# Kernel tuning notes

Measured on AMD Instinct MI355X. Metric: run time of the kernel, lower is better.

## Reference

```python
import jax, jax.numpy as jnp
import numpy as np


def _trilinear_sample(src, flow):
    """Faithful port of VoxelMorph SpatialTransformer: identity grid + flow,
    trilinear grid_sample with align_corners=True and zero padding.
    Normalization to [-1,1] followed by grid_sample's un-normalization
    (align_corners=True) is the identity, so we sample directly at voxel
    coordinates grid + flow.  src: [B,C,D,H,W], flow: [B,3,D,H,W]."""
    B, C, D, H, W = src.shape
    gz, gy, gx = jnp.meshgrid(jnp.arange(D, dtype=src.dtype),
                              jnp.arange(H, dtype=src.dtype),
                              jnp.arange(W, dtype=src.dtype), indexing='ij')
    z = gz[None] + flow[:, 0]  # [B,D,H,W] sample coords along dim0
    y = gy[None] + flow[:, 1]
    x = gx[None] + flow[:, 2]

    z0 = jnp.floor(z); y0 = jnp.floor(y); x0 = jnp.floor(x)
    fz = z - z0; fy = y - y0; fx = x - x0
    z0i = z0.astype(jnp.int32); y0i = y0.astype(jnp.int32); x0i = x0.astype(jnp.int32)

    N = D * H * W
    src_flat = src.reshape(B, C, N)
    gather = jax.vmap(lambda sf, li: sf[:, li])  # per-batch gather over flat spatial

    out = jnp.zeros((B, C, N), dtype=src.dtype)
    for dz in (0, 1):
        wz = fz if dz else (1.0 - fz)
        zi = z0i + dz
        for dy in (0, 1):
            wy = fy if dy else (1.0 - fy)
            yi = y0i + dy
            for dx in (0, 1):
                wx = fx if dx else (1.0 - fx)
                xi = x0i + dx
                # zero padding: out-of-bounds corners contribute nothing
                valid = ((zi >= 0) & (zi < D) & (yi >= 0) & (yi < H) &
                         (xi >= 0) & (xi < W))
                zc = jnp.clip(zi, 0, D - 1)
                yc = jnp.clip(yi, 0, H - 1)
                xc = jnp.clip(xi, 0, W - 1)
                lin = ((zc * H + yc) * W + xc).reshape(B, N)
                w = (wz * wy * wx * valid.astype(src.dtype)).reshape(B, 1, N)
                out = out + w * gather(src_flat, lin)  # [B,C,N]
    return out.reshape(B, C, D, H, W)


def setup_inputs() -> dict:
    key = jax.random.key(0)
    k1, k2 = jax.random.split(key)
    src = jax.random.normal(k1, (2, 2, 160, 192, 160), dtype=jnp.float32)
    flow = jax.random.normal(k2, (2, 3, 160, 192, 160), dtype=jnp.float32)
    return {"src": src, "flow": flow}


def reference(src, flow):
    return _trilinear_sample(src, flow)
```

## Files before the change

kernel.cpp:

```cpp
#include <hip/hip_runtime.h>

#define BB 2
#define CC 2
#define DD 160
#define HH 192
#define WW 160
#define HW_ (HH * WW)
#define NN (DD * HW_)

#define TX 32
#define TY 8
#define CZ 20
#define HALO 4
#define SLOTS 10
#define ROWS (TY + 2 * HALO)
#define RSTR (TX + 2 * HALO)
#define PLANE_CH (RSTR * ROWS)
#define PLANE_LDS (PLANE_CH * CC)

typedef float f2u __attribute__((ext_vector_type(2), aligned(4)));

__global__ __launch_bounds__(256) void st_warp3d_tiled(
    const float* __restrict__ src,
    const float* __restrict__ flow,
    float* __restrict__ out)
{
    const int tid = threadIdx.x;
    const int tx = tid & (TX - 1);
    const int ty = tid >> 5;

    const int tile = blockIdx.x;
    const int Xo = (tile % 5) * TX;
    const int Yo = (tile / 5) * TY;
    const int Z0 = blockIdx.y * CZ;
    const int b  = blockIdx.z;

    const int x = Xo + tx;
    const int y = Yo + ty;

    const int sxlo = max(Xo - HALO, 0);
    const int sxhi = min(Xo + TX + HALO, WW);
    const int Ws   = sxhi - sxlo;
    const int sylo = max(Yo - HALO, 0);
    const int syhi = min(Yo + TY + HALO, HH);
    const int Rs   = syhi - sylo;

    __shared__ float lds[SLOTS * PLANE_LDS];

    const float* __restrict__ sbase = src + (size_t)b * CC * NN;

    int goffA = 0, loffA = 0; bool vA;
    {
        const int s  = tid;
        const int ch = (s >= 160) ? 1 : 0;
        const int r  = s - ch * 160;
        const int yy = r / 10;
        const int xs = r - yy * 10;
        vA    = (yy < Rs) && (xs * 4 < Ws);
        goffA = ch * NN + (sylo + yy) * WW + sxlo + xs * 4;
        loffA = ch * PLANE_CH + yy * RSTR + xs * 4;
    }
    int goffB = 0, loffB = 0; bool vB = false;
    if (tid < 64) {
        const int s  = tid + 256;
        const int r  = s - 160;
        const int yy = r / 10;
        const int xs = r - yy * 10;
        vB    = (yy < Rs) && (xs * 4 < Ws);
        goffB = NN + (sylo + yy) * WW + sxlo + xs * 4;
        loffB = PLANE_CH + yy * RSTR + xs * 4;
    }

    const int qlo  = max(Z0 - HALO, 0);
    const int qhi0 = min(Z0 + HALO, DD - 1);
    for (int qq = qlo; qq <= qhi0; ++qq) {
        const float* gp = sbase + (size_t)qq * HW_;
        float* lp = lds + (qq % SLOTS) * PLANE_LDS;
        if (vA) *(float4*)(lp + loffA) = *(const float4*)(gp + goffA);
        if (vB) *(float4*)(lp + loffB) = *(const float4*)(gp + goffB);
    }
    const int qmax = min(DD - 1, Z0 + CZ - 1 + HALO);

    const size_t fbase = (size_t)b * 3 * NN + (size_t)y * WW + x;
    const size_t obase = (size_t)b * CC * NN + (size_t)y * WW + x;

    for (int z = Z0; z < Z0 + CZ; ++z) {
        __syncthreads();

        const int qp = z + HALO + 1;
        const bool pre = (qp <= qmax);
        float4 pA, pB;
        if (pre) {
            const float* gp = sbase + (size_t)qp * HW_;
            if (vA) pA = *(const float4*)(gp + goffA);
            if (vB) pB = *(const float4*)(gp + goffB);
        }

        const float* fl = flow + fbase + (size_t)z * HW_;
        const float fzv = __builtin_nontemporal_load(fl);
        const float fyv = __builtin_nontemporal_load(fl + NN);
        const float fxv = __builtin_nontemporal_load(fl + 2 * (size_t)NN);
        const float zc = (float)z + fzv;
        const float yc = (float)y + fyv;
        const float xc = (float)x + fxv;

        const float z0f = floorf(zc), y0f = floorf(yc), x0f = floorf(xc);
        const float fz = zc - z0f, fy = yc - y0f, fx = xc - x0f;
        const int z0 = (int)z0f, y0 = (int)y0f, x0 = (int)x0f;
        const int z1 = z0 + 1, y1 = y0 + 1, x1 = x0 + 1;

        const float wz0 = (z0 >= 0 && z0 < DD) ? (1.0f - fz) : 0.0f;
        const float wz1 = (z1 >= 0 && z1 < DD) ? fz : 0.0f;
        const float wy0 = (y0 >= 0 && y0 < HH) ? (1.0f - fy) : 0.0f;
        const float wy1 = (y1 >= 0 && y1 < HH) ? fy : 0.0f;
        const float wx0 = (x0 >= 0 && x0 < WW) ? (1.0f - fx) : 0.0f;
        const float wx1 = (x1 >= 0 && x1 < WW) ? fx : 0.0f;

        const int z0c = min(max(z0, 0), DD - 1), z1c = min(max(z1, 0), DD - 1);
        const int y0c = min(max(y0, 0), HH - 1), y1c = min(max(y1, 0), HH - 1);
        const int x0c = min(max(x0, 0), WW - 1), x1c = min(max(x1, 0), WW - 1);
        const int xb  = min(max(x0, 0), WW - 2);

        const float q0 = (x0c == xb ? wx0 : 0.0f) + (x1c == xb ? wx1 : 0.0f);
        const float q1 = (wx0 + wx1) - q0;
        const float w00 = wz0 * wy0, w01 = wz0 * wy1, w10 = wz1 * wy0, w11 = wz1 * wy1;
        const float w00q0 = w00 * q0, w00q1 = w00 * q1;
        const float w01q0 = w01 * q0, w01q1 = w01 * q1;
        const float w10q0 = w10 * q0, w10q1 = w10 * q1;
        const float w11q0 = w11 * q0, w11q1 = w11 * q1;

        const int dzi = z0 - z, dyi = y0 - y, dxi = x0 - x;
        const bool inTile = ((unsigned)(dzi + HALO) <= 7u) &&
                            ((unsigned)(dyi + HALO) <= 7u) &&
                            ((unsigned)(dxi + HALO) <= 7u);

        float acc0, acc1;
        if (inTile) {
            const int slot0 = z0c % SLOTS;
            const int slot1 = z1c % SLOTS;
            const int yi0 = y0c - sylo, yi1 = y1c - sylo;
            const int xi  = xb - sxlo;
            const int i00 = slot0 * PLANE_LDS + yi0 * RSTR + xi;
            const int i01 = slot0 * PLANE_LDS + yi1 * RSTR + xi;
            const int i10 = slot1 * PLANE_LDS + yi0 * RSTR + xi;
            const int i11 = slot1 * PLANE_LDS + yi1 * RSTR + xi;

            const float a00x = lds[i00],            a00y = lds[i00 + 1];
            const float a01x = lds[i01],            a01y = lds[i01 + 1];
            const float a10x = lds[i10],            a10y = lds[i10 + 1];
            const float a11x = lds[i11],            a11y = lds[i11 + 1];
            const float b00x = lds[i00 + PLANE_CH], b00y = lds[i00 + PLANE_CH + 1];
            const float b01x = lds[i01 + PLANE_CH], b01y = lds[i01 + PLANE_CH + 1];
            const float b10x = lds[i10 + PLANE_CH], b10y = lds[i10 + PLANE_CH + 1];
            const float b11x = lds[i11 + PLANE_CH], b11y = lds[i11 + PLANE_CH + 1];

            acc0 = a00x * w00q0 + a00y * w00q1 + a01x * w01q0 + a01y * w01q1 +
                   a10x * w10q0 + a10y * w10q1 + a11x * w11q0 + a11y * w11q1;
            acc1 = b00x * w00q0 + b00y * w00q1 + b01x * w01q0 + b01y * w01q1 +
                   b10x * w10q0 + b10y * w10q1 + b11x * w11q0 + b11y * w11q1;
        } else {
            const int r00 = (z0c * HH + y0c) * WW + xb;
            const int r01 = (z0c * HH + y1c) * WW + xb;
            const int r10 = (z1c * HH + y0c) * WW + xb;
            const int r11 = (z1c * HH + y1c) * WW + xb;
            const float* s1p = sbase + NN;
            const f2u a00 = *(const f2u*)(sbase + r00);
            const f2u a01 = *(const f2u*)(sbase + r01);
            const f2u a10 = *(const f2u*)(sbase + r10);
            const f2u a11 = *(const f2u*)(sbase + r11);
            const f2u c00 = *(const f2u*)(s1p + r00);
            const f2u c01 = *(const f2u*)(s1p + r01);
            const f2u c10 = *(const f2u*)(s1p + r10);
            const f2u c11 = *(const f2u*)(s1p + r11);
            acc0 = a00.x * w00q0 + a00.y * w00q1 + a01.x * w01q0 + a01.y * w01q1 +
                   a10.x * w10q0 + a10.y * w10q1 + a11.x * w11q0 + a11.y * w11q1;
            acc1 = c00.x * w00q0 + c00.y * w00q1 + c01.x * w01q0 + c01.y * w01q1 +
                   c10.x * w10q0 + c10.y * w10q1 + c11.x * w11q0 + c11.y * w11q1;
        }

        float* o = out + obase + (size_t)z * HW_;
        __builtin_nontemporal_store(acc0, o);
        __builtin_nontemporal_store(acc1, o + NN);

        if (pre) {
            float* lp = lds + (qp % SLOTS) * PLANE_LDS;
            if (vA) *(float4*)(lp + loffA) = pA;
            if (vB) *(float4*)(lp + loffB) = pB;
        }
    }
}

extern "C" void kernel_launch(void* const* d_in, const int* in_sizes, int n_in,
                              void* d_out, int out_size, void* d_ws, size_t ws_size,
                              hipStream_t stream) {
    const float* src  = (const float*)d_in[0];
    const float* flow = (const float*)d_in[1];
    float* out = (float*)d_out;

    dim3 grid(5 * 24, DD / CZ, BB);
    dim3 block(256);
    st_warp3d_tiled<<<grid, block, 0, stream>>>(src, flow, out);
}
```

Measured before the change: 290.6 us.

## Enlarge tile to 32x16, use anisotropic halo, and deepen plane prefetch pipeline

Doubles the tile height to 16 rows with 512 threads, shrinks the Y halo to 3 while keeping X/Z halos at 4, and adds an extra LDS slot so the next source plane is written at the top of each iteration while the following plane is loaded into registers. The larger tile reduces halo overhead per output and the one-iteration-deeper prefetch hides global load latency across the barrier. The in-tile test is rewritten to compare against the actual loaded bounds, so samples with displacement beyond the smaller Y halo fall back to global gathers more often.

```diff
diff --git a/kernel.cpp b/kernel.cpp
--- a/kernel.cpp
+++ b/kernel.cpp
@@ -9,18 +9,20 @@
 #define NN (DD * HW_)
 
 #define TX 32
-#define TY 8
+#define TY 16
 #define CZ 20
-#define HALO 4
-#define SLOTS 10
-#define ROWS (TY + 2 * HALO)
-#define RSTR (TX + 2 * HALO)
+#define HX 4
+#define HY 3
+#define HZ 4
+#define SLOTS 11
+#define ROWS (TY + 2 * HY)
+#define RSTR (TX + 2 * HX)
 #define PLANE_CH (RSTR * ROWS)
 #define PLANE_LDS (PLANE_CH * CC)
 
 typedef float f2u __attribute__((ext_vector_type(2), aligned(4)));
 
-__global__ __launch_bounds__(256) void st_warp3d_tiled(
+__global__ __launch_bounds__(512, 4) void st_warp3d_tiled2(
     const float* __restrict__ src,
     const float* __restrict__ flow,
     float* __restrict__ out)
@@ -38,48 +40,38 @@
     const int x = Xo + tx;
     const int y = Yo + ty;
 
-    const int sxlo = max(Xo - HALO, 0);
-    const int sxhi = min(Xo + TX + HALO, WW);
+    const int sxlo = max(Xo - HX, 0);
+    const int sxhi = min(Xo + TX + HX, WW);
     const int Ws   = sxhi - sxlo;
-    const int sylo = max(Yo - HALO, 0);
-    const int syhi = min(Yo + TY + HALO, HH);
+    const int sylo = max(Yo - HY, 0);
+    const int syhi = min(Yo + TY + HY, HH);
     const int Rs   = syhi - sylo;
 
     __shared__ float lds[SLOTS * PLANE_LDS];
-
     const float* __restrict__ sbase = src + (size_t)b * CC * NN;
 
-    int goffA = 0, loffA = 0; bool vA;
+    int goff = 0, loff = 0; bool vA = false;
     {
-        const int s  = tid;
-        const int ch = (s >= 160) ? 1 : 0;
-        const int r  = s - ch * 160;
+        const int ch = tid >> 8;
+        const int r  = tid & 255;
         const int yy = r / 10;
         const int xs = r - yy * 10;
-        vA    = (yy < Rs) && (xs * 4 < Ws);
-        goffA = ch * NN + (sylo + yy) * WW + sxlo + xs * 4;
-        loffA = ch * PLANE_CH + yy * RSTR + xs * 4;
-    }
-    int goffB = 0, loffB = 0; bool vB = false;
-    if (tid < 64) {
-        const int s  = tid + 256;
-        const int r  = s - 160;
-        const int yy = r / 10;
-        const int xs = r - yy * 10;
-        vB    = (yy < Rs) && (xs * 4 < Ws);
-        goffB = NN + (sylo + yy) * WW + sxlo + xs * 4;
-        loffB = PLANE_CH + yy * RSTR + xs * 4;
+        vA   = (r < ROWS * 10) && (yy < Rs) && (xs * 4 < Ws);
+        goff = ch * NN + (sylo + yy) * WW + sxlo + xs * 4;
+        loff = ch * PLANE_CH + yy * RSTR + xs * 4;
     }
 
-    const int qlo  = max(Z0 - HALO, 0);
-    const int qhi0 = min(Z0 + HALO, DD - 1);
-    for (int qq = qlo; qq <= qhi0; ++qq) {
-        const float* gp = sbase + (size_t)qq * HW_;
-        float* lp = lds + (qq % SLOTS) * PLANE_LDS;
-        if (vA) *(float4*)(lp + loffA) = *(const float4*)(gp + goffA);
-        if (vB) *(float4*)(lp + loffB) = *(const float4*)(gp + goffB);
+    const int qmax = min(DD - 1, Z0 + CZ - 1 + HZ + 1);
+    for (int q = max(Z0 - HZ, 0); q <= min(Z0 + HZ + 1, DD - 1); ++q) {
+        if (vA) *(float4*)(lds + (q % SLOTS) * PLANE_LDS + loff) =
+                *(const float4*)(sbase + (size_t)q * HW_ + goff);
     }
-    const int qmax = min(DD - 1, Z0 + CZ - 1 + HALO);
+    float4 preg{};
+    {
+        const int p0 = Z0 + HZ + 2;
+        if (p0 <= qmax && vA)
+            preg = *(const float4*)(sbase + (size_t)p0 * HW_ + goff);
+    }
 
     const size_t fbase = (size_t)b * 3 * NN + (size_t)y * WW + x;
     const size_t obase = (size_t)b * CC * NN + (size_t)y * WW + x;
@@ -87,14 +79,13 @@
     for (int z = Z0; z < Z0 + CZ; ++z) {
         __syncthreads();
 
-        const int qp = z + HALO + 1;
-        const bool pre = (qp <= qmax);
-        float4 pA, pB;
-        if (pre) {
-            const float* gp = sbase + (size_t)qp * HW_;
-            if (vA) pA = *(const float4*)(gp + goffA);
-            if (vB) pB = *(const float4*)(gp + goffB);
-        }
+        const int wp = z + HZ + 2;
+        if (wp <= qmax && vA)
+            *(float4*)(lds + (wp % SLOTS) * PLANE_LDS + loff) = preg;
+
+        const int np = wp + 1;
+        if (np <= qmax && vA)
+            preg = *(const float4*)(sbase + (size_t)np * HW_ + goff);
 
         const float* fl = flow + fbase + (size_t)z * HW_;
         const float fzv = __builtin_nontemporal_load(fl);
@@ -129,15 +120,15 @@
         const float w10q0 = w10 * q0, w10q1 = w10 * q1;
         const float w11q0 = w11 * q0, w11q1 = w11 * q1;
 
-        const int dzi = z0 - z, dyi = y0 - y, dxi = x0 - x;
-        const bool inTile = ((unsigned)(dzi + HALO) <= 7u) &&
-                            ((unsigned)(dyi + HALO) <= 7u) &&
-                            ((unsigned)(dxi + HALO) <= 7u);
+        const bool inTile = (z0c >= z - HZ) & (z1c <= z + HZ + 1) &
+                            (y0c >= sylo) & (y1c < syhi) &
+                            (xb >= sxlo) & (xb < sxhi - 1);
 
         float acc0, acc1;
         if (inTile) {
             const int slot0 = z0c % SLOTS;
-            const int slot1 = z1c % SLOTS;
+            int slot1 = slot0 + (z1c - z0c);
+            slot1 = (slot1 == SLOTS) ? 0 : slot1;
             const int yi0 = y0c - sylo, yi1 = y1c - sylo;
             const int xi  = xb - sxlo;
             const int i00 = slot0 * PLANE_LDS + yi0 * RSTR + xi;
@@ -181,12 +172,6 @@
         float* o = out + obase + (size_t)z * HW_;
         __builtin_nontemporal_store(acc0, o);
         __builtin_nontemporal_store(acc1, o + NN);
-
-        if (pre) {
-            float* lp = lds + (qp % SLOTS) * PLANE_LDS;
-            if (vA) *(float4*)(lp + loffA) = pA;
-            if (vB) *(float4*)(lp + loffB) = pB;
-        }
     }
 }
 
@@ -197,7 +182,7 @@
     const float* flow = (const float*)d_in[1];
     float* out = (float*)d_out;
 
-    dim3 grid(5 * 24, DD / CZ, BB);
-    dim3 block(256);
-    st_warp3d_tiled<<<grid, block, 0, stream>>>(src, flow, out);
+    dim3 grid(5 * 12, DD / CZ, BB);
+    dim3 block(TX * TY);
+    st_warp3d_tiled2<<<grid, block, 0, stream>>>(src, flow, out);
 }
```

After: 267.6 us. 1.09x faster.
